# Optimization experiments

Hardware: AMD Instinct MI355X
Metric: run time of the kernel (lower is better)

The kernel has to match this reference:

```python
import jax, jax.numpy as jnp
import numpy as np

T, B, I, H = 512, 64, 256, 512


def setup_inputs() -> dict:
    key = jax.random.key(0)
    ks = jax.random.split(key, 17)
    s_in = 1.0 / np.sqrt(I)  # nn.Linear default init bound
    s_h = 1.0 / np.sqrt(H)

    def u(k, shape, s):
        return jax.random.uniform(k, shape, jnp.float32, -s, s)

    inp = {"x": jax.random.normal(ks[0], (T, B, I), jnp.float32)}
    idx = 1
    for n in ["f", "i", "o", "c"]:
        inp[f"W{n}"] = u(ks[idx], (H, I), s_in); idx += 1
        inp[f"bW{n}"] = u(ks[idx], (H,), s_in); idx += 1
    for n in ["f", "i", "o", "c"]:
        inp[f"U{n}"] = u(ks[idx], (H, H), s_h); idx += 1
        inp[f"bU{n}"] = u(ks[idx], (H,), s_h); idx += 1
    return inp


def reference(x, Wf, bWf, Wi, bWi, Wo, bWo, Wc, bWc,
              Uf, bUf, Ui, bUi, Uo, bUo, Uc, bUc):
    Hd = Wf.shape[0]
    # Fuse the 4 input-projection GEMMs into one big (T*B, I) x (I, 4H) GEMM,
    # folding both bias sets in (same math as Wg(x_t)+Ug(h) per gate).
    Wall = jnp.concatenate([Wf, Wi, Wo, Wc], axis=0)          # (4H, I)
    Uall = jnp.concatenate([Uf, Ui, Uo, Uc], axis=0)          # (4H, H)
    ball = jnp.concatenate([bWf + bUf, bWi + bUi, bWo + bUo, bWc + bUc], axis=0)
    xW = jnp.einsum('tbi,gi->tbg', x, Wall) + ball            # (T, B, 4H)

    def step(carry, xw_t):
        h, c = carry                                          # (B, H) each
        g = xw_t + h @ Uall.T                                 # (B, 4H)
        f = jax.nn.sigmoid(g[:, :Hd])
        i = jax.nn.sigmoid(g[:, Hd:2 * Hd])
        o = jax.nn.sigmoid(g[:, 2 * Hd:3 * Hd])
        c = f * c + i * jnp.tanh(g[:, 3 * Hd:])
        h = o * jnp.tanh(c)
        return (h, c), h

    Bsz = x.shape[1]
    h0 = jnp.zeros((Bsz, Hd), x.dtype)
    c0 = jnp.zeros((Bsz, Hd), x.dtype)
    (h, c), h_seq = jax.lax.scan(step, (h0, c0), xW)
    # torch code cats (1,B,H) tensors along 0 -> (T,B,H); final states keep (1,B,H)
    return h_seq, h[None], c[None]
```

## Files before the change

kernel.cpp:

```cpp
#include <hip/hip_runtime.h>
#include <cstdint>
#include <cstddef>


typedef __attribute__((ext_vector_type(8))) short short8;
typedef __attribute__((ext_vector_type(4))) float float4v;

__device__ __forceinline__ unsigned short f2bf(float f) {
  unsigned u = __float_as_uint(f);
  u = u + 0x7FFFu + ((u >> 16) & 1u);
  return (unsigned short)(u >> 16);
}
__device__ __forceinline__ float bf2f(unsigned short s) {
  return __uint_as_float(((unsigned)s) << 16);
}
__device__ __forceinline__ unsigned long long pack4(float4 v) {
  return (unsigned long long)f2bf(v.x) |
         ((unsigned long long)f2bf(v.y) << 16) |
         ((unsigned long long)f2bf(v.z) << 32) |
         ((unsigned long long)f2bf(v.w) << 48);
}

__global__ void prep_kernel(
    const float* __restrict__ Wf, const float* __restrict__ bWf,
    const float* __restrict__ Wi, const float* __restrict__ bWi,
    const float* __restrict__ Wo, const float* __restrict__ bWo,
    const float* __restrict__ Wc, const float* __restrict__ bWc,
    const float* __restrict__ Uf, const float* __restrict__ bUf,
    const float* __restrict__ Ui, const float* __restrict__ bUi,
    const float* __restrict__ Uo, const float* __restrict__ bUo,
    const float* __restrict__ Uc, const float* __restrict__ bUc,
    unsigned short* __restrict__ Wall, unsigned short* __restrict__ Uall,
    float* __restrict__ ball, int* __restrict__ flags)
{
  const float* Ws[4]  = {Wf, Wi, Wo, Wc};
  const float* Us[4]  = {Uf, Ui, Uo, Uc};
  const float* bWs[4] = {bWf, bWi, bWo, bWc};
  const float* bUs[4] = {bUf, bUi, bUo, bUc};
  const long long NW4 = 131072;
  const long long NU4 = 262144;
  const long long NB4 = 512;
  const long long TOT = NW4 + NU4 + NB4;
  long long idx0 = (long long)blockIdx.x * blockDim.x + threadIdx.x;
  if (idx0 < 64) flags[idx0] = 0;
  long long stride = (long long)gridDim.x * blockDim.x;
  for (long long u = idx0; u < TOT; u += stride) {
    if (u < NW4) {
      int e = (int)(u << 2);
      int n = e >> 8, k = e & 255;
      float4 v = *(const float4*)(Ws[n >> 9] + (size_t)(n & 511) * 256 + k);
      ((unsigned long long*)Wall)[u] = pack4(v);
    } else if (u < NW4 + NU4) {
      long long q = u - NW4;
      int e = (int)(q << 2);
      int n = e >> 9, k = e & 511;
      float4 v = *(const float4*)(Us[n >> 9] + (size_t)(n & 511) * 512 + k);
      ((unsigned long long*)Uall)[q] = pack4(v);
    } else {
      long long q = u - NW4 - NU4;
      int e = (int)(q << 2);
      int gate = e >> 9, r = e & 511;
      float4 a = *(const float4*)(bWs[gate] + r);
      float4 b = *(const float4*)(bUs[gate] + r);
      float4 sv;
      sv.x = a.x + b.x; sv.y = a.y + b.y; sv.z = a.z + b.z; sv.w = a.w + b.w;
      *(float4*)(ball + e) = sv;
    }
  }
}

__global__ __launch_bounds__(256, 2) void xw_gemm(
    const float* __restrict__ x,
    const unsigned short* __restrict__ Wall,
    const float* __restrict__ ball,
    unsigned short* __restrict__ xw)
{
  __shared__ short As[128 * 72];
  __shared__ short Bs[128 * 72];
  const int tid = threadIdx.x;
  const int bn = blockIdx.x, bm = blockIdx.y;
  const int Mbase = bm * 128, Nbase = bn * 128;
  const int w = tid >> 6, L = tid & 63, lq = L >> 4, lr = L & 15;
  const int wm = w >> 1, wn = w & 1;
  const int srow = tid >> 1, shalf = tid & 1;

  float4v acc[4][4];
  #pragma unroll
  for (int a = 0; a < 4; ++a)
    #pragma unroll
    for (int b = 0; b < 4; ++b) acc[a][b] = (float4v){0.f, 0.f, 0.f, 0.f};

  for (int ko = 0; ko < 256; ko += 64) {
    const float* gaf = x + (size_t)(Mbase + srow) * 256 + ko + shalf * 32;
    float4 f0 = *(const float4*)(gaf);
    float4 f1 = *(const float4*)(gaf + 4);
    float4 f2 = *(const float4*)(gaf + 8);
    float4 f3 = *(const float4*)(gaf + 12);
    float4 f4 = *(const float4*)(gaf + 16);
    float4 f5 = *(const float4*)(gaf + 20);
    float4 f6 = *(const float4*)(gaf + 24);
    float4 f7 = *(const float4*)(gaf + 28);
    const unsigned short* gb = Wall + (size_t)(Nbase + srow) * 256 + ko + shalf * 32;
    short8 b0 = *(const short8*)(gb);
    short8 b1 = *(const short8*)(gb + 8);
    short8 b2 = *(const short8*)(gb + 16);
    short8 b3 = *(const short8*)(gb + 24);
    __syncthreads();
    {
      unsigned long long* pa = (unsigned long long*)&As[srow * 72 + shalf * 32];
      pa[0] = pack4(f0); pa[1] = pack4(f1);
      pa[2] = pack4(f2); pa[3] = pack4(f3);
      pa[4] = pack4(f4); pa[5] = pack4(f5);
      pa[6] = pack4(f6); pa[7] = pack4(f7);
      short* pb = &Bs[srow * 72 + shalf * 32];
      *(short8*)(pb) = b0; *(short8*)(pb + 8) = b1;
      *(short8*)(pb + 16) = b2; *(short8*)(pb + 24) = b3;
    }
    __syncthreads();
    #pragma unroll
    for (int kk = 0; kk < 64; kk += 32) {
      short8 af[4], bfr[4];
      #pragma unroll
      for (int mi = 0; mi < 4; ++mi)
        af[mi] = *(const short8*)&As[(wm * 64 + mi * 16 + lr) * 72 + kk + lq * 8];
      #pragma unroll
      for (int ni = 0; ni < 4; ++ni)
        bfr[ni] = *(const short8*)&Bs[(wn * 64 + ni * 16 + lr) * 72 + kk + lq * 8];
      #pragma unroll
      for (int mi = 0; mi < 4; ++mi)
        #pragma unroll
        for (int ni = 0; ni < 4; ++ni)
          acc[mi][ni] = __builtin_amdgcn_mfma_f32_16x16x32_bf16(
              af[mi], bfr[ni], acc[mi][ni], 0, 0, 0);
    }
  }
  #pragma unroll
  for (int ni = 0; ni < 4; ++ni) {
    int col = Nbase + wn * 64 + ni * 16 + lr;
    float bias = ball[col];
    #pragma unroll
    for (int mi = 0; mi < 4; ++mi) {
      #pragma unroll
      for (int r = 0; r < 4; ++r) {
        int row = Mbase + wm * 64 + mi * 16 + lq * 4 + r;
        xw[(size_t)row * 2048 + col] = f2bf(acc[mi][ni][r] + bias);
      }
    }
  }
}

__global__ __launch_bounds__(256, 1) void lstm_scan(
    const unsigned short* __restrict__ xw,
    const unsigned short* __restrict__ Uall,
    unsigned short* __restrict__ hbuf,
    int* __restrict__ flags,
    float* __restrict__ out)
{
  __shared__ short hstage[16 * 520];
  __shared__ float gates[4 * 16 * 33];
  __shared__ unsigned short xwb[4 * 16 * 32];

  const int tid = threadIdx.x;
  const int wg = blockIdx.x;
  const int g = wg >> 4;
  const int s = wg & 15;
  const int w = tid >> 6, L = tid & 63, lq = L >> 4, lr = L & 15;

  const int eb = tid >> 4;
  const int ej = (tid & 15) * 2;
  const int xb = tid >> 4, xg = (tid >> 2) & 3, xc = tid & 3;

  float* hseq = out;
  float* hfin = out + (size_t)512 * 64 * 512;
  float* cfin = hfin + (size_t)64 * 512;
  int* grp_flags = flags + g * 16;

  short8 uf[2][16];
  #pragma unroll
  for (int nt = 0; nt < 2; ++nt)
    #pragma unroll
    for (int kt = 0; kt < 16; ++kt) {
      const unsigned short* p = Uall +
          (size_t)(w * 512 + s * 32 + nt * 16 + lr) * 512 + kt * 32 + lq * 8;
      uf[nt][kt] = *(const short8*)p;
    }

  float c0 = 0.f, c1 = 0.f, h0 = 0.f, h1 = 0.f;

  for (int t = 0; t < 512; ++t) {
    const unsigned short* xp = xw +
        ((size_t)(t * 64 + g * 16 + xb)) * 2048 + xg * 512 + s * 32 + xc * 8;
    short8 xv = *(const short8*)xp;

    float4v a0a = (float4v){0.f, 0.f, 0.f, 0.f};
    float4v a0b = (float4v){0.f, 0.f, 0.f, 0.f};
    float4v a1a = (float4v){0.f, 0.f, 0.f, 0.f};
    float4v a1b = (float4v){0.f, 0.f, 0.f, 0.f};

    if (t > 0) {
      if (tid < 16) {
        while (__hip_atomic_load(&grp_flags[tid], __ATOMIC_RELAXED,
                                 __HIP_MEMORY_SCOPE_AGENT) < t)
          __builtin_amdgcn_s_sleep(1);
      }
      __syncthreads();
      const unsigned short* hsrc =
          hbuf + ((size_t)((t - 1) & 1)) * 32768 + (size_t)g * 8192;
      const int scol = (tid & 63) * 8;
      const int sr0 = tid >> 6;
      unsigned long long hv[8];
      #pragma unroll
      for (int r = 0; r < 4; ++r) {
        const unsigned long long* p = (const unsigned long long*)
            (hsrc + (size_t)(sr0 + r * 4) * 512 + scol);
        hv[2 * r]     = __hip_atomic_load(p, __ATOMIC_RELAXED,
                                          __HIP_MEMORY_SCOPE_AGENT);
        hv[2 * r + 1] = __hip_atomic_load(p + 1, __ATOMIC_RELAXED,
                                          __HIP_MEMORY_SCOPE_AGENT);
      }
      #pragma unroll
      for (int r = 0; r < 4; ++r) {
        unsigned long long* q =
            (unsigned long long*)&hstage[(sr0 + r * 4) * 520 + scol];
        q[0] = hv[2 * r]; q[1] = hv[2 * r + 1];
      }
      __syncthreads();
      #pragma unroll
      for (int kt = 0; kt < 8; ++kt) {
        short8 afA = *(const short8*)&hstage[lr * 520 + kt * 32 + lq * 8];
        short8 afB = *(const short8*)&hstage[lr * 520 + (kt + 8) * 32 + lq * 8];
        a0a = __builtin_amdgcn_mfma_f32_16x16x32_bf16(afA, uf[0][kt], a0a, 0, 0, 0);
        a0b = __builtin_amdgcn_mfma_f32_16x16x32_bf16(afB, uf[0][kt + 8], a0b, 0, 0, 0);
        a1a = __builtin_amdgcn_mfma_f32_16x16x32_bf16(afA, uf[1][kt], a1a, 0, 0, 0);
        a1b = __builtin_amdgcn_mfma_f32_16x16x32_bf16(afB, uf[1][kt + 8], a1b, 0, 0, 0);
      }
    }
    float4v acc0 = a0a + a0b;
    float4v acc1 = a1a + a1b;

    #pragma unroll
    for (int r = 0; r < 4; ++r) {
      gates[w * 528 + (lq * 4 + r) * 33 + lr] = acc0[r];
      gates[w * 528 + (lq * 4 + r) * 33 + 16 + lr] = acc1[r];
    }
    *(short8*)&xwb[xg * 512 + xb * 32 + xc * 8] = xv;
    __syncthreads();

    {
      float gf = gates[eb * 33 + ej] + bf2f(xwb[eb * 32 + ej]);
      float gi = gates[528 + eb * 33 + ej] + bf2f(xwb[512 + eb * 32 + ej]);
      float go = gates[1056 + eb * 33 + ej] + bf2f(xwb[1024 + eb * 32 + ej]);
      float gc = gates[1584 + eb * 33 + ej] + bf2f(xwb[1536 + eb * 32 + ej]);
      float f_ = 1.f / (1.f + __expf(-gf));
      float i_ = 1.f / (1.f + __expf(-gi));
      float o_ = 1.f / (1.f + __expf(-go));
      float ct = 1.f - 2.f / (__expf(2.f * gc) + 1.f);
      c0 = f_ * c0 + i_ * ct;
      h0 = o_ * (1.f - 2.f / (__expf(2.f * c0) + 1.f));
    }
    {
      int j = ej + 1;
      float gf = gates[eb * 33 + j] + bf2f(xwb[eb * 32 + j]);
      float gi = gates[528 + eb * 33 + j] + bf2f(xwb[512 + eb * 32 + j]);
      float go = gates[1056 + eb * 33 + j] + bf2f(xwb[1024 + eb * 32 + j]);
      float gc = gates[1584 + eb * 33 + j] + bf2f(xwb[1536 + eb * 32 + j]);
      float f_ = 1.f / (1.f + __expf(-gf));
      float i_ = 1.f / (1.f + __expf(-gi));
      float o_ = 1.f / (1.f + __expf(-go));
      float ct = 1.f - 2.f / (__expf(2.f * gc) + 1.f);
      c1 = f_ * c1 + i_ * ct;
      h1 = o_ * (1.f - 2.f / (__expf(2.f * c1) + 1.f));
    }
    unsigned hb = ((unsigned)f2bf(h1) << 16) | (unsigned)f2bf(h0);
    unsigned* hdst = (unsigned*)(hbuf + ((size_t)(t & 1)) * 32768 +
                                 ((size_t)(g * 16 + eb)) * 512 + s * 32 + ej);
    __hip_atomic_store(hdst, hb, __ATOMIC_RELAXED, __HIP_MEMORY_SCOPE_AGENT);

    __syncthreads();
    if (tid == 0)
      __hip_atomic_store(&grp_flags[s], t + 1, __ATOMIC_RELAXED,
                         __HIP_MEMORY_SCOPE_AGENT);

    size_t orow = ((size_t)(t * 64 + g * 16 + eb)) * 512 + s * 32 + ej;
    {
      float2 hv2 = make_float2(h0, h1);
      __builtin_nontemporal_store(*(double*)&hv2, (double*)(hseq + orow));
    }
  }

  size_t fo = ((size_t)(g * 16 + eb)) * 512 + s * 32 + ej;
  *(float2*)(hfin + fo) = make_float2(h0, h1);
  *(float2*)(cfin + fo) = make_float2(c0, c1);
}

extern "C" void kernel_launch(void* const* d_in, const int* in_sizes, int n_in,
                              void* d_out, int out_size, void* d_ws, size_t ws_size,
                              hipStream_t stream) {
  (void)in_sizes; (void)n_in; (void)out_size; (void)ws_size;
  const float* x   = (const float*)d_in[0];
  const float* Wf  = (const float*)d_in[1];
  const float* bWf = (const float*)d_in[2];
  const float* Wi  = (const float*)d_in[3];
  const float* bWi = (const float*)d_in[4];
  const float* Wo  = (const float*)d_in[5];
  const float* bWo = (const float*)d_in[6];
  const float* Wc  = (const float*)d_in[7];
  const float* bWc = (const float*)d_in[8];
  const float* Uf  = (const float*)d_in[9];
  const float* bUf = (const float*)d_in[10];
  const float* Ui  = (const float*)d_in[11];
  const float* bUi = (const float*)d_in[12];
  const float* Uo  = (const float*)d_in[13];
  const float* bUo = (const float*)d_in[14];
  const float* Uc  = (const float*)d_in[15];
  const float* bUc = (const float*)d_in[16];

  char* ws = (char*)d_ws;
  unsigned short* xw   = (unsigned short*)(ws);
  unsigned short* Wall = (unsigned short*)(ws + 134217728);
  unsigned short* Uall = (unsigned short*)(ws + 135266304);
  float*          ball = (float*)         (ws + 137363456);
  unsigned short* hbuf = (unsigned short*)(ws + 137371648);
  int*            flags= (int*)           (ws + 137502720);

  prep_kernel<<<768, 256, 0, stream>>>(Wf, bWf, Wi, bWi, Wo, bWo, Wc, bWc,
                                       Uf, bUf, Ui, bUi, Uo, bUo, Uc, bUc,
                                       Wall, Uall, ball, flags);
  xw_gemm<<<dim3(16, 256), 256, 0, stream>>>(x, Wall, ball, xw);
  lstm_scan<<<64, 256, 0, stream>>>(xw, Uall, hbuf, flags, (float*)d_out);
}
```

Measured before the change: 1.511 ms.

## Load h fragments directly from global per wave, drop LDS staging and barriers

Each wave now spins on the group flags itself and loads its MFMA A-fragments of the previous hidden state straight from global memory into registers. This removes the LDS staging buffer and two block-wide __syncthreads per timestep on the serial recurrence path. In exchange, all four waves redundantly fetch the same 16x512 h tile from L2, which raises global traffic and register pressure. Each wave also polls the flags separately, adding more atomic polling.

```diff
diff --git a/kernel.cpp b/kernel.cpp
--- a/kernel.cpp
+++ b/kernel.cpp
@@ -5,6 +5,8 @@
 
 typedef __attribute__((ext_vector_type(8))) short short8;
 typedef __attribute__((ext_vector_type(4))) float float4v;
+
+typedef union { unsigned long long u[2]; short8 s8; } frag_t;
 
 __device__ __forceinline__ unsigned short f2bf(float f) {
   unsigned u = __float_as_uint(f);
@@ -156,7 +158,6 @@
     int* __restrict__ flags,
     float* __restrict__ out)
 {
-  __shared__ short hstage[16 * 520];
   __shared__ float gates[4 * 16 * 33];
   __shared__ unsigned short xwb[4 * 16 * 32];
 
@@ -198,41 +199,36 @@
     float4v a1b = (float4v){0.f, 0.f, 0.f, 0.f};
 
     if (t > 0) {
-      if (tid < 16) {
-        while (__hip_atomic_load(&grp_flags[tid], __ATOMIC_RELAXED,
+      if (L < 16) {
+        while (__hip_atomic_load(&grp_flags[L], __ATOMIC_RELAXED,
                                  __HIP_MEMORY_SCOPE_AGENT) < t)
           __builtin_amdgcn_s_sleep(1);
       }
-      __syncthreads();
-      const unsigned short* hsrc =
-          hbuf + ((size_t)((t - 1) & 1)) * 32768 + (size_t)g * 8192;
-      const int scol = (tid & 63) * 8;
-      const int sr0 = tid >> 6;
-      unsigned long long hv[8];
-      #pragma unroll
-      for (int r = 0; r < 4; ++r) {
-        const unsigned long long* p = (const unsigned long long*)
-            (hsrc + (size_t)(sr0 + r * 4) * 512 + scol);
-        hv[2 * r]     = __hip_atomic_load(p, __ATOMIC_RELAXED,
-                                          __HIP_MEMORY_SCOPE_AGENT);
-        hv[2 * r + 1] = __hip_atomic_load(p + 1, __ATOMIC_RELAXED,
-                                          __HIP_MEMORY_SCOPE_AGENT);
+      const unsigned long long* hrow = (const unsigned long long*)
+          (hbuf + ((size_t)((t - 1) & 1)) * 32768 +
+           ((size_t)(g * 16 + lr)) * 512);
+      frag_t fa[8], fb[8];
+      #pragma unroll
+      for (int kt = 0; kt < 8; ++kt) {
+        fa[kt].u[0] = __hip_atomic_load(hrow + kt * 8 + lq * 2,
+                                        __ATOMIC_RELAXED,
+                                        __HIP_MEMORY_SCOPE_AGENT);
+        fa[kt].u[1] = __hip_atomic_load(hrow + kt * 8 + lq * 2 + 1,
+                                        __ATOMIC_RELAXED,
+                                        __HIP_MEMORY_SCOPE_AGENT);
+        fb[kt].u[0] = __hip_atomic_load(hrow + 64 + kt * 8 + lq * 2,
+                                        __ATOMIC_RELAXED,
+                                        __HIP_MEMORY_SCOPE_AGENT);
+        fb[kt].u[1] = __hip_atomic_load(hrow + 64 + kt * 8 + lq * 2 + 1,
+                                        __ATOMIC_RELAXED,
+                                        __HIP_MEMORY_SCOPE_AGENT);
       }
       #pragma unroll
-      for (int r = 0; r < 4; ++r) {
-        unsigned long long* q =
-            (unsigned long long*)&hstage[(sr0 + r * 4) * 520 + scol];
-        q[0] = hv[2 * r]; q[1] = hv[2 * r + 1];
-      }
-      __syncthreads();
-      #pragma unroll
       for (int kt = 0; kt < 8; ++kt) {
-        short8 afA = *(const short8*)&hstage[lr * 520 + kt * 32 + lq * 8];
-        short8 afB = *(const short8*)&hstage[lr * 520 + (kt + 8) * 32 + lq * 8];
-        a0a = __builtin_amdgcn_mfma_f32_16x16x32_bf16(afA, uf[0][kt], a0a, 0, 0, 0);
-        a0b = __builtin_amdgcn_mfma_f32_16x16x32_bf16(afB, uf[0][kt + 8], a0b, 0, 0, 0);
-        a1a = __builtin_amdgcn_mfma_f32_16x16x32_bf16(afA, uf[1][kt], a1a, 0, 0, 0);
-        a1b = __builtin_amdgcn_mfma_f32_16x16x32_bf16(afB, uf[1][kt + 8], a1b, 0, 0, 0);
+        a0a = __builtin_amdgcn_mfma_f32_16x16x32_bf16(fa[kt].s8, uf[0][kt], a0a, 0, 0, 0);
+        a0b = __builtin_amdgcn_mfma_f32_16x16x32_bf16(fb[kt].s8, uf[0][kt + 8], a0b, 0, 0, 0);
+        a1a = __builtin_amdgcn_mfma_f32_16x16x32_bf16(fa[kt].s8, uf[1][kt], a1a, 0, 0, 0);
+        a1b = __builtin_amdgcn_mfma_f32_16x16x32_bf16(fb[kt].s8, uf[1][kt + 8], a1b, 0, 0, 0);
       }
     }
     float4v acc0 = a0a + a0b;
```

After: 2.884 ms. 1.91x slower.
